# Kernel optimization log

Measured on AMD Instinct MI355X. Metric: run time of the kernel, lower is better.

Reference implementation:

```python
import jax, jax.numpy as jnp
import numpy as np

N_NODES = 50000
N_EDGES = 600000
HIDDEN = 128
N_FEAT = 1
N_CLASSES = 2
N_GRAPHS = 500


def gcn_conv(x, W, b, src, dst, n_nodes):
    # PyG GCNConv: add self-loops, symmetric normalization deg^{-1/2} A_hat deg^{-1/2}, then XW + b
    h = x @ W  # [N, out]
    deg = jnp.zeros((n_nodes,), h.dtype).at[dst].add(1.0) + 1.0  # +1 for self-loop
    dinv = jax.lax.rsqrt(deg)
    norm = dinv[src] * dinv[dst]  # [E]
    agg = jax.ops.segment_sum(h[src] * norm[:, None], dst, num_segments=n_nodes)
    # self-loop contribution: norm_ii = dinv_i^2
    agg = agg + h * (dinv * dinv)[:, None]
    return agg + b


def setup_inputs() -> dict:
    key = jax.random.key(0)
    ks = jax.random.split(key, 12)
    x = jax.random.normal(ks[0], (N_NODES, N_FEAT), dtype=jnp.float32)
    edge_index = jax.random.randint(ks[1], (2, N_EDGES), 0, N_NODES, dtype=jnp.int64)
    batch = jnp.sort(jax.random.randint(ks[2], (N_NODES,), 0, N_GRAPHS, dtype=jnp.int64))

    def glorot(k, fan_in, fan_out):
        lim = np.sqrt(6.0 / (fan_in + fan_out)).astype(np.float32)
        return jax.random.uniform(k, (fan_in, fan_out), jnp.float32, -lim, lim)

    W1 = glorot(ks[3], N_FEAT, HIDDEN)
    b1 = jnp.zeros((HIDDEN,), jnp.float32)
    W2 = glorot(ks[4], HIDDEN, HIDDEN)
    b2 = jnp.zeros((HIDDEN,), jnp.float32)
    W3 = glorot(ks[5], HIDDEN, HIDDEN)
    b3 = jnp.zeros((HIDDEN,), jnp.float32)
    Wlin = glorot(ks[6], HIDDEN, N_CLASSES)
    blin = jnp.zeros((N_CLASSES,), jnp.float32)
    return {"x": x, "W1": W1, "b1": b1, "W2": W2, "b2": b2, "W3": W3,
            "b3": b3, "Wlin": Wlin, "blin": blin,
            "edge_index": edge_index, "batch": batch}


def reference(x, W1, b1, W2, b2, W3, b3, Wlin, blin, edge_index, batch):
    src, dst = edge_index[0], edge_index[1]
    n = x.shape[0]
    h = jax.nn.relu(gcn_conv(x, W1, b1, src, dst, n))
    h = jax.nn.relu(gcn_conv(h, W2, b2, src, dst, n))
    h = gcn_conv(h, W3, b3, src, dst, n)
    # global mean pool over graphs
    sums = jax.ops.segment_sum(h, batch, num_segments=N_GRAPHS)
    counts = jax.ops.segment_sum(jnp.ones((n,), h.dtype), batch, num_segments=N_GRAPHS)
    pooled = sums / jnp.maximum(counts, 1.0)[:, None]  # [G, HIDDEN]
    # dropout is identity in eval mode
    return pooled @ Wlin + blin  # [G, N_CLASSES]
```

## Files before the change

### kernel.cpp

```cpp
#include <hip/hip_runtime.h>

#define N_NODES 50000
#define N_EDGES 600000
#define HID     128
#define NG      500
#define NB_SCAN 196
#define MAXDEG  48
#define ECAP    664
#define EBLK    586

typedef __attribute__((ext_vector_type(8))) short short8;
typedef __attribute__((ext_vector_type(4))) float f32x4;

static __device__ __forceinline__ ushort f2bf(float f) {
    uint u = __float_as_uint(f);
    return (ushort)((u + 0x7fffu + ((u >> 16) & 1u)) >> 16);
}
static __device__ __forceinline__ float bf2f(ushort h) {
    return __uint_as_float(((uint)h) << 16);
}


__global__ void k_ellfill(const int* __restrict__ src, const int* __restrict__ dst,
                          int* __restrict__ cnt, int* __restrict__ ell_t,
                          const float* __restrict__ W2, const float* __restrict__ W3,
                          const float* __restrict__ Wlin, const float* __restrict__ b3,
                          const float* __restrict__ blin, const int* __restrict__ batch,
                          float* __restrict__ w3buf, ushort* __restrict__ w2fh,
                          ushort* __restrict__ w2fl, int* __restrict__ starts) {
    if (blockIdx.x >= EBLK) {
        int t = threadIdx.x;
        if (blockIdx.x == EBLK) {
            int k = t >> 1, j = t & 1;
            float acc = 0.f;
            for (int m = 0; m < 128; m++) acc += W3[k * 128 + m] * Wlin[m * 2 + j];
            w3buf[k * 2 + j] = acc;
            if (t < 2) {
                float c = 0.f;
                for (int m = 0; m < 128; m++) c += b3[m] * Wlin[m * 2 + t];
                w3buf[256 + t] = c + blin[t];
                w3buf[258 + t] = blin[t];
            }
        } else {
            for (int idx = t; idx < 16384; idx += 256) {
                int nt = idx >> 11, kt = (idx >> 9) & 3, ln = (idx >> 3) & 63, i = idx & 7;
                int k = kt * 32 + (ln >> 4) * 8 + i;
                int col = nt * 16 + (ln & 15);
                float v = W2[k * 128 + col];
                ushort h = f2bf(v);
                w2fh[idx] = h;
                w2fl[idx] = f2bf(v - bf2f(h));
            }
            for (int g = t; g <= NG; g += 256) {
                int lo = 0, hi = N_NODES;
                while (lo < hi) { int mid = (lo + hi) >> 1; if (batch[mid] < g) lo = mid + 1; else hi = mid; }
                starts[g] = lo;
            }
        }
        return;
    }
    int base = blockIdx.x * 1024 + threadIdx.x;
    #pragma unroll
    for (int u = 0; u < 4; u++) {
        int e = base + u * 256;
        if (e < N_EDGES) {
            int d = dst[e];
            int p = atomicAdd(&cnt[d], 1);
            if (p < MAXDEG) ell_t[p * N_NODES + d] = src[e];
        }
    }
}

__global__ void k_nodeprep(const int* __restrict__ cnt, const float* __restrict__ x,
                           float* __restrict__ dinv, float* __restrict__ xd) {
    int i = blockIdx.x * 256 + threadIdx.x;
    if (i < N_NODES) {
        float di = rsqrtf((float)cnt[i] + 1.0f);
        dinv[i] = di;
        xd[i] = x[i] * di;
    }
}

__global__ void k_s1d(const float* __restrict__ x, const float* __restrict__ xd,
                      const float* __restrict__ dinv, const int* __restrict__ cnt,
                      const int* __restrict__ ell_t, float2* __restrict__ s1d) {
    int tid = blockIdx.x * 256 + threadIdx.x;
    int i = tid >> 2, sub = tid & 3;
    if (i >= N_NODES) return;
    int c = min(cnt[i], MAXDEG);
    float acc = 0.f;
    for (int p = sub; p < c; p += 4) acc += xd[ell_t[p * N_NODES + i]];
    acc += __shfl_xor(acc, 1);
    acc += __shfl_xor(acc, 2);
    if (sub == 0) {
        float di = dinv[i];
        float2 r = {x[i] * di * di + acc * di, di};
        s1d[i] = r;
    }
}


__global__ __launch_bounds__(256, 8) void k_gemm_fused(const float2* __restrict__ s1d,
                                                       const int* __restrict__ cnt,
                                                       const int* __restrict__ ell_t,
                                                       const float* __restrict__ W1,
                                                       const float* __restrict__ b1,
                                                       const ushort* __restrict__ w2fh,
                                                       const ushort* __restrict__ w2fl,
                                                       const float* __restrict__ b2,
                                                       const float* __restrict__ w3buf,
                                                       const float* __restrict__ dinv,
                                                       float* __restrict__ zd) {
    __shared__ __align__(16) ushort Hhi[32 * 136];
    __shared__ __align__(16) ushort Hlo[32 * 136];
    __shared__ float2 sjd_sh[ECAP];
    __shared__ int cnt_sh[32];
    __shared__ int pref_sh[33];
    __shared__ int maxc_sh;
    int t = threadIdx.x;
    int r0 = blockIdx.x * 32;
    int lane = t & 31, grp = t >> 5;

    if (t < 32) {
        int i = r0 + t;
        int c = (i < N_NODES) ? min(cnt[i], MAXDEG) : 0;
        cnt_sh[t] = c;
        int inc = c, mx = c;
        for (int o = 1; o < 32; o <<= 1) {
            int u = __shfl_up(inc, o);
            if (t >= o) inc += u;
            mx = max(mx, __shfl_xor(mx, o));
        }
        pref_sh[t] = inc - c;
        if (t == 31) { pref_sh[32] = inc; maxc_sh = mx; }
    }
    __syncthreads();
    int total = pref_sh[32];
    int maxc  = maxc_sh;
    bool fast = (total <= ECAP);
    if (fast) {
        for (int slot = t; slot < 32 * maxc; slot += 256) {
            int p = slot >> 5, ln = slot & 31;
            if (p < cnt_sh[ln]) {
                int j = ell_t[p * N_NODES + r0 + ln];
                sjd_sh[pref_sh[ln] + p] = s1d[j];
            }
        }
    }
    __syncthreads();

    float w1r[16], b1r[16];
    #pragma unroll
    for (int kk = 0; kk < 16; kk++) { w1r[kk] = W1[grp * 16 + kk]; b1r[kk] = b1[grp * 16 + kk]; }

    float ga[16];
    #pragma unroll
    for (int kk = 0; kk < 16; kk++) ga[kk] = 0.f;
    int node = r0 + lane;
    if (node < N_NODES) {
        float2 sd = s1d[node];
        float di = sd.y, wself = sd.y * sd.y;
        #pragma unroll
        for (int kk = 0; kk < 16; kk++) ga[kk] = fmaxf(sd.x * w1r[kk] + b1r[kk], 0.f) * wself;
        int c = cnt_sh[lane];
        if (fast) {
            const float2* myrow = &sjd_sh[pref_sh[lane]];
            int p = 0;
            for (; p + 3 < c; p += 4) {
                float2 s0 = myrow[p], s1v = myrow[p+1], s2 = myrow[p+2], s3 = myrow[p+3];
                float wj0 = s0.y * di, wj1 = s1v.y * di, wj2 = s2.y * di, wj3 = s3.y * di;
                #pragma unroll
                for (int kk = 0; kk < 16; kk++) {
                    ga[kk] += fmaxf(s0.x  * w1r[kk] + b1r[kk], 0.f) * wj0
                            + fmaxf(s1v.x * w1r[kk] + b1r[kk], 0.f) * wj1
                            + fmaxf(s2.x  * w1r[kk] + b1r[kk], 0.f) * wj2
                            + fmaxf(s3.x  * w1r[kk] + b1r[kk], 0.f) * wj3;
                }
            }
            for (; p < c; p++) {
                float2 sj = myrow[p];
                float wj = sj.y * di;
                #pragma unroll
                for (int kk = 0; kk < 16; kk++)
                    ga[kk] += fmaxf(sj.x * w1r[kk] + b1r[kk], 0.f) * wj;
            }
        } else {
            for (int p = 0; p < c; p++) {
                float2 sj = s1d[ell_t[p * N_NODES + node]];
                float wj = sj.y * di;
                #pragma unroll
                for (int kk = 0; kk < 16; kk++)
                    ga[kk] += fmaxf(sj.x * w1r[kk] + b1r[kk], 0.f) * wj;
            }
        }
    }
    #pragma unroll
    for (int kk = 0; kk < 16; kk += 2) {
        int ch = grp * 16 + kk;
        ushort h0 = f2bf(ga[kk]);      ushort l0 = f2bf(ga[kk]     - bf2f(h0));
        ushort h1v = f2bf(ga[kk + 1]); ushort l1v = f2bf(ga[kk + 1] - bf2f(h1v));
        *(uint*)&Hhi[lane * 136 + ch] = (uint)h0 | ((uint)h1v << 16);
        *(uint*)&Hlo[lane * 136 + ch] = (uint)l0 | ((uint)l1v << 16);
    }
    __syncthreads();

    int wv = t >> 6, l = t & 63;
    int l15 = l & 15, lk = l >> 4;
    f32x4 acc00 = {0.f,0.f,0.f,0.f}, acc01 = {0.f,0.f,0.f,0.f};
    f32x4 acc10 = {0.f,0.f,0.f,0.f}, acc11 = {0.f,0.f,0.f,0.f};
    const short8* Bh = (const short8*)w2fh;
    const short8* Bl = (const short8*)w2fl;
    #pragma unroll
    for (int kt = 0; kt < 4; kt++) {
        int ao = l15 * 136 + kt * 32 + lk * 8;
        short8 ah0 = *(const short8*)&Hhi[ao];
        short8 ah1 = *(const short8*)&Hhi[ao + 16 * 136];
        short8 al0 = *(const short8*)&Hlo[ao];
        short8 al1 = *(const short8*)&Hlo[ao + 16 * 136];
        {
            int ng = 2 * wv;
            short8 bh = Bh[(ng * 4 + kt) * 64 + l];
            short8 bl = Bl[(ng * 4 + kt) * 64 + l];
            acc00 = __builtin_amdgcn_mfma_f32_16x16x32_bf16(ah0, bh, acc00, 0, 0, 0);
            acc00 = __builtin_amdgcn_mfma_f32_16x16x32_bf16(ah0, bl, acc00, 0, 0, 0);
            acc00 = __builtin_amdgcn_mfma_f32_16x16x32_bf16(al0, bh, acc00, 0, 0, 0);
            acc10 = __builtin_amdgcn_mfma_f32_16x16x32_bf16(ah1, bh, acc10, 0, 0, 0);
            acc10 = __builtin_amdgcn_mfma_f32_16x16x32_bf16(ah1, bl, acc10, 0, 0, 0);
            acc10 = __builtin_amdgcn_mfma_f32_16x16x32_bf16(al1, bh, acc10, 0, 0, 0);
        }
        {
            int ng = 2 * wv + 1;
            short8 bh = Bh[(ng * 4 + kt) * 64 + l];
            short8 bl = Bl[(ng * 4 + kt) * 64 + l];
            acc01 = __builtin_amdgcn_mfma_f32_16x16x32_bf16(ah0, bh, acc01, 0, 0, 0);
            acc01 = __builtin_amdgcn_mfma_f32_16x16x32_bf16(ah0, bl, acc01, 0, 0, 0);
            acc01 = __builtin_amdgcn_mfma_f32_16x16x32_bf16(al0, bh, acc01, 0, 0, 0);
            acc11 = __builtin_amdgcn_mfma_f32_16x16x32_bf16(ah1, bh, acc11, 0, 0, 0);
            acc11 = __builtin_amdgcn_mfma_f32_16x16x32_bf16(ah1, bl, acc11, 0, 0, 0);
            acc11 = __builtin_amdgcn_mfma_f32_16x16x32_bf16(al1, bh, acc11, 0, 0, 0);
        }
    }

    float p0[2][4], p1[2][4];
    #pragma unroll
    for (int mt = 0; mt < 2; mt++)
        #pragma unroll
        for (int r = 0; r < 4; r++) { p0[mt][r] = 0.f; p1[mt][r] = 0.f; }
    {
        int colg = (2 * wv) * 16 + l15;
        float b2c = b2[colg], w0 = w3buf[colg * 2], w1c = w3buf[colg * 2 + 1];
        #pragma unroll
        for (int r = 0; r < 4; r++) {
            float v0 = fmaxf(acc00[r] + b2c, 0.f);
            float v1 = fmaxf(acc10[r] + b2c, 0.f);
            p0[0][r] += v0 * w0; p1[0][r] += v0 * w1c;
            p0[1][r] += v1 * w0; p1[1][r] += v1 * w1c;
        }
    }
    {
        int colg = (2 * wv + 1) * 16 + l15;
        float b2c = b2[colg], w0 = w3buf[colg * 2], w1c = w3buf[colg * 2 + 1];
        #pragma unroll
        for (int r = 0; r < 4; r++) {
            float v0 = fmaxf(acc01[r] + b2c, 0.f);
            float v1 = fmaxf(acc11[r] + b2c, 0.f);
            p0[0][r] += v0 * w0; p1[0][r] += v0 * w1c;
            p0[1][r] += v1 * w0; p1[1][r] += v1 * w1c;
        }
    }
    #pragma unroll
    for (int o = 1; o < 16; o <<= 1) {
        #pragma unroll
        for (int mt = 0; mt < 2; mt++)
            #pragma unroll
            for (int r = 0; r < 4; r++) {
                p0[mt][r] += __shfl_xor(p0[mt][r], o);
                p1[mt][r] += __shfl_xor(p1[mt][r], o);
            }
    }
    float* zpart = (float*)sjd_sh;
    if (l15 == 0) {
        #pragma unroll
        for (int mt = 0; mt < 2; mt++)
            #pragma unroll
            for (int r = 0; r < 4; r++) {
                int row = mt * 16 + lk * 4 + r;
                zpart[(wv * 32 + row) * 2 + 0] = p0[mt][r];
                zpart[(wv * 32 + row) * 2 + 1] = p1[mt][r];
            }
    }
    __syncthreads();
    if (t < 64) {
        int row = t >> 1, o = t & 1;
        float s = zpart[row * 2 + o] + zpart[(32 + row) * 2 + o]
                + zpart[(64 + row) * 2 + o] + zpart[(96 + row) * 2 + o];
        int rg = r0 + row;
        if (rg < N_NODES) zd[rg * 2 + o] = s * dinv[rg];
    }
}


__global__ void k_aggz(const float* __restrict__ zd, const int* __restrict__ cnt,
                       const int* __restrict__ ell_t, const float* __restrict__ dinv,
                       float2* __restrict__ az) {
    int tid = blockIdx.x * 256 + threadIdx.x;
    int i = tid >> 2, sub = tid & 3;
    if (i >= N_NODES) return;
    const float2* Z = (const float2*)zd;
    int c = min(cnt[i], MAXDEG);
    float a0 = 0.f, a1 = 0.f;
    for (int p = sub; p < c; p += 4) {
        float2 zj = Z[ell_t[p * N_NODES + i]];
        a0 += zj.x; a1 += zj.y;
    }
    a0 += __shfl_xor(a0, 1); a1 += __shfl_xor(a1, 1);
    a0 += __shfl_xor(a0, 2); a1 += __shfl_xor(a1, 2);
    if (sub == 0) {
        float di = dinv[i];
        float2 zi = Z[i];
        float2 r = {(zi.x + a0) * di, (zi.y + a1) * di};
        az[i] = r;
    }
}


__global__ __launch_bounds__(64) void k_final(const float2* __restrict__ az,
                                              const int* __restrict__ starts,
                                              const float* __restrict__ w3buf,
                                              float* __restrict__ out) {
    int g = blockIdx.x;
    int lane = threadIdx.x;
    int start = starts[g], end = starts[g + 1];
    float a0 = 0.f, a1 = 0.f;
    for (int n = start + lane; n < end; n += 64) {
        float2 v = az[n];
        a0 += v.x; a1 += v.y;
    }
    for (int o = 32; o; o >>= 1) { a0 += __shfl_xor(a0, o); a1 += __shfl_xor(a1, o); }
    if (lane == 0) {
        if (end > start) {
            float inv = 1.0f / (float)(end - start);
            out[g * 2 + 0] = a0 * inv + w3buf[256];
            out[g * 2 + 1] = a1 * inv + w3buf[257];
        } else {
            out[g * 2 + 0] = w3buf[258];
            out[g * 2 + 1] = w3buf[259];
        }
    }
}


extern "C" void kernel_launch(void* const* d_in, const int* in_sizes, int n_in,
                              void* d_out, int out_size, void* d_ws, size_t ws_size,
                              hipStream_t stream) {
    const float* x    = (const float*)d_in[0];
    const float* W1   = (const float*)d_in[1];
    const float* b1   = (const float*)d_in[2];
    const float* W2   = (const float*)d_in[3];
    const float* b2   = (const float*)d_in[4];
    const float* W3   = (const float*)d_in[5];
    const float* b3   = (const float*)d_in[6];
    const float* Wlin = (const float*)d_in[7];
    const float* blin = (const float*)d_in[8];
    const int*   eidx = (const int*)d_in[9];
    const int*   batch= (const int*)d_in[10];
    const int* esrc = eidx;
    const int* edst = eidx + N_EDGES;
    float* out = (float*)d_out;

    char* w = (char*)d_ws;
    size_t off = 0;
    auto alloc = [&](size_t bytes) { size_t o = off; off = (off + bytes + 255) & ~(size_t)255; return o; };
    int*   cnt    = (int*)  (w + alloc(N_NODES * 4));
    int*   ell_t  = (int*)  (w + alloc((size_t)N_NODES * MAXDEG * 4));
    float* dinv   = (float*)(w + alloc(N_NODES * 4));
    float* xd     = (float*)(w + alloc(N_NODES * 4));
    float2* s1d   = (float2*)(w + alloc((size_t)N_NODES * 8));
    float* w3buf  = (float*)(w + alloc(260 * 4));
    float* zd     = (float*)(w + alloc((size_t)N_NODES * 2 * 4));
    float2* az    = (float2*)(w + alloc((size_t)N_NODES * 8));
    ushort* w2fh  = (ushort*)(w + alloc(16384 * 2));
    ushort* w2fl  = (ushort*)(w + alloc(16384 * 2));
    int*   starts = (int*)  (w + alloc((NG + 4) * 4));

    const int QB = (N_NODES * 4 + 255) / 256;
    hipMemsetAsync(cnt, 0, N_NODES * 4, stream);
    k_ellfill<<<EBLK + 2, 256, 0, stream>>>(esrc, edst, cnt, ell_t, W2, W3, Wlin, b3, blin,
                                            batch, w3buf, w2fh, w2fl, starts);
    k_nodeprep<<<NB_SCAN, 256, 0, stream>>>(cnt, x, dinv, xd);
    k_s1d<<<QB, 256, 0, stream>>>(x, xd, dinv, cnt, ell_t, s1d);
    k_gemm_fused<<<(N_NODES + 31) / 32, 256, 0, stream>>>(s1d, cnt, ell_t,
                                                          W1, b1, w2fh, w2fl, b2, w3buf,
                                                          dinv, zd);
    k_aggz<<<QB, 256, 0, stream>>>(zd, cnt, ell_t, dinv, az);
    k_final<<<NG, 64, 0, stream>>>(az, starts, w3buf, out);
}
```

Measured before the change: 160.0 us.

## Switch ELL adjacency to row-major layout and widen per-node gather lanes

The ELL neighbor table moves from a transposed slot-major layout to a node-major layout, so each node's neighbor list is contiguous. The gather kernels k_s1d and k_aggz now use 8 lanes per node instead of 4, and the staging loop in k_gemm_fused is a fixed 6-iteration unrolled loop over contiguous rows. The W2 split conversion and the batch-start binary search are spread over more auxiliary blocks. The aim is better-coalesced index reads in the consumers. The cost is scattered 4-byte writes in the atomic ELL fill and many idle lanes for low-degree nodes.

```diff
diff --git a/kernel.cpp b/kernel.cpp
--- a/kernel.cpp
+++ b/kernel.cpp
@@ -22,7 +22,7 @@
 
 
 __global__ void k_ellfill(const int* __restrict__ src, const int* __restrict__ dst,
-                          int* __restrict__ cnt, int* __restrict__ ell_t,
+                          int* __restrict__ cnt, int* __restrict__ ell,
                           const float* __restrict__ W2, const float* __restrict__ W3,
                           const float* __restrict__ Wlin, const float* __restrict__ b3,
                           const float* __restrict__ blin, const int* __restrict__ batch,
@@ -41,8 +41,14 @@
                 w3buf[256 + t] = c + blin[t];
                 w3buf[258 + t] = blin[t];
             }
+            for (int g = t; g <= NG; g += 256) {
+                int lo = 0, hi = N_NODES;
+                while (lo < hi) { int mid = (lo + hi) >> 1; if (batch[mid] < g) lo = mid + 1; else hi = mid; }
+                starts[g] = lo;
+            }
         } else {
-            for (int idx = t; idx < 16384; idx += 256) {
+            int q = blockIdx.x - (EBLK + 1);
+            for (int idx = q * 4096 + t; idx < (q + 1) * 4096; idx += 256) {
                 int nt = idx >> 11, kt = (idx >> 9) & 3, ln = (idx >> 3) & 63, i = idx & 7;
                 int k = kt * 32 + (ln >> 4) * 8 + i;
                 int col = nt * 16 + (ln & 15);
@@ -51,11 +57,6 @@
                 w2fh[idx] = h;
                 w2fl[idx] = f2bf(v - bf2f(h));
             }
-            for (int g = t; g <= NG; g += 256) {
-                int lo = 0, hi = N_NODES;
-                while (lo < hi) { int mid = (lo + hi) >> 1; if (batch[mid] < g) lo = mid + 1; else hi = mid; }
-                starts[g] = lo;
-            }
         }
         return;
     }
@@ -66,7 +67,7 @@
         if (e < N_EDGES) {
             int d = dst[e];
             int p = atomicAdd(&cnt[d], 1);
-            if (p < MAXDEG) ell_t[p * N_NODES + d] = src[e];
+            if (p < MAXDEG) ell[d * MAXDEG + p] = src[e];
         }
     }
 }
@@ -83,15 +84,16 @@
 
 __global__ void k_s1d(const float* __restrict__ x, const float* __restrict__ xd,
                       const float* __restrict__ dinv, const int* __restrict__ cnt,
-                      const int* __restrict__ ell_t, float2* __restrict__ s1d) {
+                      const int* __restrict__ ell, float2* __restrict__ s1d) {
     int tid = blockIdx.x * 256 + threadIdx.x;
-    int i = tid >> 2, sub = tid & 3;
+    int i = tid >> 3, sub = tid & 7;
     if (i >= N_NODES) return;
     int c = min(cnt[i], MAXDEG);
     float acc = 0.f;
-    for (int p = sub; p < c; p += 4) acc += xd[ell_t[p * N_NODES + i]];
+    for (int p = sub; p < c; p += 8) acc += xd[ell[i * MAXDEG + p]];
     acc += __shfl_xor(acc, 1);
     acc += __shfl_xor(acc, 2);
+    acc += __shfl_xor(acc, 4);
     if (sub == 0) {
         float di = dinv[i];
         float2 r = {x[i] * di * di + acc * di, di};
@@ -102,7 +104,7 @@
 
 __global__ __launch_bounds__(256, 8) void k_gemm_fused(const float2* __restrict__ s1d,
                                                        const int* __restrict__ cnt,
-                                                       const int* __restrict__ ell_t,
+                                                       const int* __restrict__ ell,
                                                        const float* __restrict__ W1,
                                                        const float* __restrict__ b1,
                                                        const ushort* __restrict__ w2fh,
@@ -116,7 +118,6 @@
     __shared__ float2 sjd_sh[ECAP];
     __shared__ int cnt_sh[32];
     __shared__ int pref_sh[33];
-    __shared__ int maxc_sh;
     int t = threadIdx.x;
     int r0 = blockIdx.x * 32;
     int lane = t & 31, grp = t >> 5;
@@ -125,24 +126,24 @@
         int i = r0 + t;
         int c = (i < N_NODES) ? min(cnt[i], MAXDEG) : 0;
         cnt_sh[t] = c;
-        int inc = c, mx = c;
+        int inc = c;
         for (int o = 1; o < 32; o <<= 1) {
             int u = __shfl_up(inc, o);
             if (t >= o) inc += u;
-            mx = max(mx, __shfl_xor(mx, o));
         }
         pref_sh[t] = inc - c;
-        if (t == 31) { pref_sh[32] = inc; maxc_sh = mx; }
+        if (t == 31) pref_sh[32] = inc;
     }
     __syncthreads();
     int total = pref_sh[32];
-    int maxc  = maxc_sh;
     bool fast = (total <= ECAP);
     if (fast) {
-        for (int slot = t; slot < 32 * maxc; slot += 256) {
-            int p = slot >> 5, ln = slot & 31;
+        #pragma unroll
+        for (int u = 0; u < 6; u++) {
+            int s = u * 256 + t;
+            int ln = s / MAXDEG, p = s - ln * MAXDEG;
             if (p < cnt_sh[ln]) {
-                int j = ell_t[p * N_NODES + r0 + ln];
+                int j = ell[(r0 + ln) * MAXDEG + p];
                 sjd_sh[pref_sh[ln] + p] = s1d[j];
             }
         }
@@ -186,7 +187,7 @@
             }
         } else {
             for (int p = 0; p < c; p++) {
-                float2 sj = s1d[ell_t[p * N_NODES + node]];
+                float2 sj = s1d[ell[node * MAXDEG + p]];
                 float wj = sj.y * di;
                 #pragma unroll
                 for (int kk = 0; kk < 16; kk++)
@@ -301,20 +302,21 @@
 
 
 __global__ void k_aggz(const float* __restrict__ zd, const int* __restrict__ cnt,
-                       const int* __restrict__ ell_t, const float* __restrict__ dinv,
+                       const int* __restrict__ ell, const float* __restrict__ dinv,
                        float2* __restrict__ az) {
     int tid = blockIdx.x * 256 + threadIdx.x;
-    int i = tid >> 2, sub = tid & 3;
+    int i = tid >> 3, sub = tid & 7;
     if (i >= N_NODES) return;
     const float2* Z = (const float2*)zd;
     int c = min(cnt[i], MAXDEG);
     float a0 = 0.f, a1 = 0.f;
-    for (int p = sub; p < c; p += 4) {
-        float2 zj = Z[ell_t[p * N_NODES + i]];
+    for (int p = sub; p < c; p += 8) {
+        float2 zj = Z[ell[i * MAXDEG + p]];
         a0 += zj.x; a1 += zj.y;
     }
     a0 += __shfl_xor(a0, 1); a1 += __shfl_xor(a1, 1);
     a0 += __shfl_xor(a0, 2); a1 += __shfl_xor(a1, 2);
+    a0 += __shfl_xor(a0, 4); a1 += __shfl_xor(a1, 4);
     if (sub == 0) {
         float di = dinv[i];
         float2 zi = Z[i];
@@ -372,7 +374,7 @@
     size_t off = 0;
     auto alloc = [&](size_t bytes) { size_t o = off; off = (off + bytes + 255) & ~(size_t)255; return o; };
     int*   cnt    = (int*)  (w + alloc(N_NODES * 4));
-    int*   ell_t  = (int*)  (w + alloc((size_t)N_NODES * MAXDEG * 4));
+    int*   ell    = (int*)  (w + alloc((size_t)N_NODES * MAXDEG * 4));
     float* dinv   = (float*)(w + alloc(N_NODES * 4));
     float* xd     = (float*)(w + alloc(N_NODES * 4));
     float2* s1d   = (float2*)(w + alloc((size_t)N_NODES * 8));
@@ -383,15 +385,15 @@
     ushort* w2fl  = (ushort*)(w + alloc(16384 * 2));
     int*   starts = (int*)  (w + alloc((NG + 4) * 4));
 
-    const int QB = (N_NODES * 4 + 255) / 256;
+    const int QB = (N_NODES * 8 + 255) / 256;
     hipMemsetAsync(cnt, 0, N_NODES * 4, stream);
-    k_ellfill<<<EBLK + 2, 256, 0, stream>>>(esrc, edst, cnt, ell_t, W2, W3, Wlin, b3, blin,
+    k_ellfill<<<EBLK + 5, 256, 0, stream>>>(esrc, edst, cnt, ell, W2, W3, Wlin, b3, blin,
                                             batch, w3buf, w2fh, w2fl, starts);
     k_nodeprep<<<NB_SCAN, 256, 0, stream>>>(cnt, x, dinv, xd);
-    k_s1d<<<QB, 256, 0, stream>>>(x, xd, dinv, cnt, ell_t, s1d);
-    k_gemm_fused<<<(N_NODES + 31) / 32, 256, 0, stream>>>(s1d, cnt, ell_t,
+    k_s1d<<<QB, 256, 0, stream>>>(x, xd, dinv, cnt, ell, s1d);
+    k_gemm_fused<<<(N_NODES + 31) / 32, 256, 0, stream>>>(s1d, cnt, ell,
                                                           W1, b1, w2fh, w2fl, b2, w3buf,
                                                           dinv, zd);
-    k_aggz<<<QB, 256, 0, stream>>>(zd, cnt, ell_t, dinv, az);
+    k_aggz<<<QB, 256, 0, stream>>>(zd, cnt, ell, dinv, az);
     k_final<<<NG, 64, 0, stream>>>(az, starts, w3buf, out);
 }
```

New measurement: 175.0 us. 9.3% more time.
